# Kernel tuning notes

Hardware: AMD Instinct MI355X
Metric: run time of the kernel (lower is better)

The kernel has to match this reference:

```python
import jax, jax.numpy as jnp
import numpy as np


def _sobel(img):
    # replicate-pad then Sobel cross-correlation (matches torch conv2d with wx, wy)
    p = jnp.pad(img, ((0, 0), (0, 0), (1, 1), (1, 1)), mode='edge')
    dx = ((p[:, :, 0:-2, 2:] - p[:, :, 0:-2, 0:-2])
          + 2.0 * (p[:, :, 1:-1, 2:] - p[:, :, 1:-1, 0:-2])
          + (p[:, :, 2:, 2:] - p[:, :, 2:, 0:-2]))
    dy = ((p[:, :, 2:, 0:-2] - p[:, :, 0:-2, 0:-2])
          + 2.0 * (p[:, :, 2:, 1:-1] - p[:, :, 0:-2, 1:-1])
          + (p[:, :, 2:, 2:] - p[:, :, 0:-2, 2:]))
    return dx, dy


def _compute_normal(vertex):
    # normal = normalize(dV/dx x dV/dy); zero out pixels at global min/max depth
    dx, dy = _sobel(vertex)
    n = jnp.cross(dx, dy, axis=1)                      # [B,3,H,W]
    mag = jnp.sqrt(jnp.sum(n * n, axis=1, keepdims=True) + 1e-16)
    n = n / (mag + 1e-8)
    depth = vertex[:, 2:3]
    invalid = (depth == depth.min()) | (depth == depth.max())
    return jnp.where(invalid, 0.0, n)


def _warp(feat, u, v):
    # bilinear sampling of feat [B,C,H,W] at (u,v) [B,N] -> [B,C,N]
    B, C, H, W = feat.shape
    u = jnp.clip(u, 0.0, W - 1.0)
    v = jnp.clip(v, 0.0, H - 1.0)
    u0 = jnp.floor(u); v0 = jnp.floor(v)
    wu = u - u0; wv = v - v0
    u0i = u0.astype(jnp.int32); v0i = v0.astype(jnp.int32)
    u1i = jnp.minimum(u0i + 1, W - 1); v1i = jnp.minimum(v0i + 1, H - 1)
    flat = feat.reshape(B, C, H * W)
    N = u.shape[-1]
    def g(ui, vi):
        idx = (vi * W + ui)[:, None, :]
        return jnp.take_along_axis(flat, jnp.broadcast_to(idx, (B, C, N)), axis=2)
    return (g(u0i, v0i) * ((1 - wu) * (1 - wv))[:, None]
            + g(u1i, v0i) * (wu * (1 - wv))[:, None]
            + g(u0i, v1i) * ((1 - wu) * wv)[:, None]
            + g(u1i, v1i) * (wu * wv)[:, None])


def _skew(v):  # [B,3] -> [B,3,3]
    x, y, z = v[..., 0], v[..., 1], v[..., 2]
    O = jnp.zeros_like(x)
    return jnp.stack([jnp.stack([O, -z, y], -1),
                      jnp.stack([z, O, -x], -1),
                      jnp.stack([-y, x, O], -1)], -2)


def _twist2mat(w):  # Rodrigues: so(3) [B,3] -> SO(3) [B,3,3]
    th = jnp.sqrt(jnp.sum(w * w, -1, keepdims=True) + 1e-24)
    Kv = _skew(w / th)
    th = th[..., None]
    I = jnp.eye(3, dtype=w.dtype)
    return I + jnp.sin(th) * Kv + (1.0 - jnp.cos(th)) * (Kv @ Kv)


def _icp_forward(depth0, depth1, K, R, t, max_iter=3):
    B, _, H, W = depth0.shape
    fx, fy, cx, cy = [K[:, i:i + 1] for i in range(4)]  # each [B,1]
    uu = jnp.arange(W, dtype=depth0.dtype)
    vv = jnp.arange(H, dtype=depth0.dtype)
    px = (uu[None, None, None, :] - cx[:, :, None, None]) / fx[:, :, None, None]
    py = (vv[None, None, :, None] - cy[:, :, None, None]) / fy[:, :, None, None]
    px = jnp.broadcast_to(px, (B, 1, H, W))
    py = jnp.broadcast_to(py, (B, 1, H, W))
    vertex0 = jnp.concatenate([px * depth0, py * depth0, depth0], 1)  # [B,3,H,W]
    vertex1 = jnp.concatenate([px * depth1, py * depth1, depth1], 1)
    normal0 = _compute_normal(vertex0)
    normal1 = _compute_normal(vertex1)
    N = H * W
    V0 = vertex0.reshape(B, 3, N)
    N0 = normal0.reshape(B, 3, N)
    P0 = V0.transpose(0, 2, 1)                          # [B,N,3]
    dpt0 = vertex0[:, 2].reshape(B, N)
    sigma_z = 0.0012 + 0.0019 * (dpt0 - 0.4) ** 2       # depth noise model
    eye6 = jnp.eye(6, dtype=depth0.dtype)
    for _ in range(max_iter):
        v0to1 = R @ V0 + t                               # [B,3,N]
        x_, y_, s_ = v0to1[:, 0], v0to1[:, 1], v0to1[:, 2]
        u_ = x_ / s_ * fx + cx
        v_ = y_ / s_ * fy + cy
        inviews = (u_ > 0) & (u_ < W - 1) & (v_ > 0) & (v_ < H - 1)
        rV1 = _warp(vertex1, u_, v_)                     # [B,3,N]
        rN1 = _warp(normal1, u_, v_)
        diff = v0to1 - rV1
        dnorm = jnp.sqrt(jnp.sum(diff * diff, axis=1) + 1e-16)
        occ = (~inviews) | (dnorm > 0.1)                 # [B,N]
        res = jnp.sum(rN1 * diff, axis=1)                # point-to-plane residual [B,N]
        NtC = jnp.einsum('bcn,bck->bnk', rN1, R)         # n_r^T R, [B,N,3]
        # n^T [p]_x == cross(n^T R, p)
        J = jnp.concatenate([jnp.cross(NtC, P0), -NtC], -1)  # [B,N,6]
        # sigma ~ |n_r . (R e_z)| * sigma_z (depth noise projected on normal)
        ndot = jnp.abs(jnp.sum(rN1 * R[:, :, 2][:, :, None], axis=1))
        sigma = ndot * sigma_z + 1e-3
        w_res = res / (sigma + 1e-8)
        J = -J / (sigma + 1e-8)[..., None]
        w_res = jnp.where(occ, 0.0, w_res)
        J = jnp.where(occ[..., None], 0.0, J)
        JtWJ = jnp.einsum('bnk,bnl->bkl', J, J)          # [B,6,6]
        JtR = jnp.einsum('bnk,bn->bk', J, w_res)[..., None]  # [B,6,1]
        tr = jnp.trace(JtWJ, axis1=1, axis2=2)
        Hlm = JtWJ + (tr * 1e-6)[:, None, None] * eye6   # LM damping
        xi = jnp.linalg.inv(Hlm) @ JtR                   # [B,6,1]
        dR = _twist2mat(-xi[:, :3, 0])
        dt = -(dR @ xi[:, 3:])
        R, t = R @ dR, R @ dt + t                        # inverse-compositional update
    weights = jnp.ones((B, 1, H, W), dtype=depth0.dtype)
    return R, t, weights


def setup_inputs() -> dict:
    key = jax.random.key(0)
    B, H, W = 16, 480, 640
    k1, k2, k3, k4 = jax.random.split(key, 4)
    TWO_PI = 6.2831853
    xs = jnp.linspace(0.0, 1.0, W, dtype=jnp.float32)
    ys = jnp.linspace(0.0, 1.0, H, dtype=jnp.float32)
    phase = jax.random.uniform(k1, (B, 1, 1, 1), minval=0.0, maxval=TWO_PI)
    # smooth positive depth surface so ICP inlier test keeps valid pixels
    depth0 = (2.0 + 0.5 * jnp.sin(TWO_PI * 3.0 * xs[None, None, None, :] + phase)
              * jnp.cos(TWO_PI * 2.0 * ys[None, None, :, None])).astype(jnp.float32)
    depth1 = depth0 + 0.01 * jax.random.normal(k2, (B, 1, H, W), dtype=jnp.float32)
    K = jnp.tile(jnp.array([[525.0, 525.0, 319.5, 239.5]], dtype=jnp.float32), (B, 1))
    w = 0.005 * jax.random.normal(k3, (B, 3), dtype=jnp.float32)
    R = _twist2mat(w)                                    # near-identity initial rotation
    t = 0.005 * jax.random.normal(k4, (B, 3, 1), dtype=jnp.float32)
    return {"depth0": depth0, "depth1": depth1, "K": K, "R": R, "t": t}


def reference(depth0, depth1, K, R, t):
    return _icp_forward(depth0, depth1, K, R, t, max_iter=3)
```

## Files before the change

### kernel.cpp

```cpp
#include <hip/hip_runtime.h>
#include <hip/hip_fp16.h>

#define IMH 480
#define IMW 640
#define HW (IMH*IMW)
#define NB 16

#define BPB 100
#define TPX 4
#define GROUPS 3
#define THREADS_PB (BPB*256)
#define GSTRIDE (THREADS_PB*TPX)
#define GROWS (GSTRIDE/IMW)

__device__ inline unsigned fenc(float x){
    unsigned u = __float_as_uint(x);
    return (u & 0x80000000u) ? ~u : (u | 0x80000000u);
}
__device__ inline float fdec(unsigned e){
    unsigned u = (e & 0x80000000u) ? (e & 0x7FFFFFFFu) : ~e;
    return __uint_as_float(u);
}

__global__ void init_kernel(const float* __restrict__ Rin, const float* __restrict__ tin,
                            float* __restrict__ stateR, float* __restrict__ statet,
                            unsigned* __restrict__ mm, float* __restrict__ acc){
    int i = threadIdx.x;
    if (i < NB*9) stateR[i] = Rin[i];
    if (i < NB*3) statet[i] = tin[i];
    if (i == 0){ mm[0] = 0xFFFFFFFFu; mm[1] = 0u; }
    for (int k = i; k < NB*27; k += 256) acc[k] = 0.f;
}

__global__ __launch_bounds__(256) void minmax_kernel(const float4* __restrict__ d, unsigned* __restrict__ mm){
    unsigned lmin = 0xFFFFFFFFu, lmax = 0u;
    const int total4 = NB*HW/4;
    for (int i = blockIdx.x*256 + threadIdx.x; i < total4; i += gridDim.x*256){
        float4 v = d[i];
        unsigned e0 = fenc(v.x), e1 = fenc(v.y), e2 = fenc(v.z), e3 = fenc(v.w);
        lmin = min(lmin, min(min(e0,e1), min(e2,e3)));
        lmax = max(lmax, max(max(e0,e1), max(e2,e3)));
    }
    #pragma unroll
    for (int off = 32; off; off >>= 1){
        lmin = min(lmin, (unsigned)__shfl_down((int)lmin, off));
        lmax = max(lmax, (unsigned)__shfl_down((int)lmax, off));
    }
    __shared__ unsigned smin[4], smax[4];
    int wave = threadIdx.x >> 6, lane = threadIdx.x & 63;
    if (lane == 0){ smin[wave] = lmin; smax[wave] = lmax; }
    __syncthreads();
    if (threadIdx.x == 0){
        unsigned bmin = min(min(smin[0],smin[1]), min(smin[2],smin[3]));
        unsigned bmax = max(max(smax[0],smax[1]), max(smax[2],smax[3]));
        atomicMin(&mm[0], bmin);
        atomicMax(&mm[1], bmax);
    }
}

__global__ __launch_bounds__(256) void normal_kernel(const float* __restrict__ depth1,
                                                     const float* __restrict__ Kp,
                                                     const unsigned* __restrict__ mm,
                                                     uint2* __restrict__ nrm,
                                                     float* __restrict__ weights){
    int b = blockIdx.y;
    int pix = blockIdx.x*256 + threadIdx.x;
    int r = pix / IMW, c = pix % IMW;
    const float fx = Kp[b*4+0], fy = Kp[b*4+1], cx = Kp[b*4+2], cy = Kp[b*4+3];
    const float inv_fx = 1.f/fx, inv_fy = 1.f/fy;
    const float* __restrict__ d = depth1 + (size_t)b*HW;
    int rm = max(r-1,0), rp = min(r+1,IMH-1), cm = max(c-1,0), cp = min(c+1,IMW-1);

    auto vert = [&](int rr, int cc, float v[3]){
        float dd = d[rr*IMW+cc];
        v[0] = ((float)cc - cx)*inv_fx*dd;
        v[1] = ((float)rr - cy)*inv_fy*dd;
        v[2] = dd;
    };
    float va[3],vb[3],vc2[3],vd[3],ve[3],vf[3],vg[3],vh[3];
    vert(rm,cm,va); vert(rm,c,vb);  vert(rm,cp,vc2);
    vert(r ,cm,vd);                 vert(r ,cp,ve);
    vert(rp,cm,vf); vert(rp,c,vg);  vert(rp,cp,vh);

    float dx[3], dy[3];
    #pragma unroll
    for (int k=0;k<3;k++){
        dx[k] = (vc2[k]-va[k]) + 2.f*(ve[k]-vd[k]) + (vh[k]-vf[k]);
        dy[k] = (vf[k]-va[k]) + 2.f*(vg[k]-vb[k]) + (vh[k]-vc2[k]);
    }
    float nx = dx[1]*dy[2] - dx[2]*dy[1];
    float ny = dx[2]*dy[0] - dx[0]*dy[2];
    float nz = dx[0]*dy[1] - dx[1]*dy[0];
    float mag = sqrtf(nx*nx + ny*ny + nz*nz + 1e-16f);
    float inv = __builtin_amdgcn_rcpf(mag + 1e-8f);
    nx *= inv; ny *= inv; nz *= inv;

    float dc = d[r*IMW+c];
    float dmin = fdec(mm[0]), dmax = fdec(mm[1]);
    if (dc == dmin || dc == dmax){ nx = 0.f; ny = 0.f; nz = 0.f; }

    __half2 hxy = __floats2half2_rn(nx, ny);
    __half2 hz0 = __floats2half2_rn(nz, 0.f);
    uint2 p;
    p.x = *reinterpret_cast<unsigned*>(&hxy);
    p.y = *reinterpret_cast<unsigned*>(&hz0);
    nrm[(size_t)b*HW + pix] = p;
    weights[(size_t)b*HW + pix] = 1.f;
}

__global__ __launch_bounds__(256) void iter_kernel(const float4* __restrict__ depth0_v4,
                                                   const float* __restrict__ depth1,
                                                   const uint2* __restrict__ nrm,
                                                   const float* __restrict__ Kp,
                                                   const float* __restrict__ stateR,
                                                   const float* __restrict__ statet,
                                                   float* __restrict__ acc){
    const int b = blockIdx.y;
    const float fx = Kp[b*4+0], fy = Kp[b*4+1], cx = Kp[b*4+2], cy = Kp[b*4+3];
    const float inv_fx = 1.f/fx, inv_fy = 1.f/fy;
    float Rm[9];
    #pragma unroll
    for (int i=0;i<9;i++) Rm[i] = stateR[b*9+i];
    float tv[3];
    #pragma unroll
    for (int i=0;i<3;i++) tv[i] = statet[b*3+i];

    const float4* __restrict__ d0v = depth0_v4 + (size_t)b*(HW/4);
    const float* __restrict__ d1   = depth1 + (size_t)b*HW;
    const uint2* __restrict__ nb_  = nrm + (size_t)b*HW;

    float accv[27];
    #pragma unroll
    for (int i=0;i<27;i++) accv[i] = 0.f;

    const int tid = blockIdx.x*256 + threadIdx.x;
    const int base0 = tid*TPX;
    const int c0 = base0 % IMW;
    const int r0 = base0 / IMW;
    const float px_base = ((float)c0 - cx)*inv_fx;
    float pyv = ((float)r0 - cy)*inv_fy;
    const float py_step = (float)GROWS*inv_fy;

    #pragma unroll 1
    for (int g = 0; g < GROUPS; g++){
        float4 d4 = d0v[tid + g*THREADS_PB];
        float dd[4] = {d4.x, d4.y, d4.z, d4.w};

        #pragma unroll
        for (int j = 0; j < TPX; j++){
            float d0 = dd[j];
            float V0x = (px_base + (float)j*inv_fx)*d0;
            float V0y = pyv*d0;
            float V0z = d0;

            float X = Rm[0]*V0x + Rm[1]*V0y + Rm[2]*V0z + tv[0];
            float Y = Rm[3]*V0x + Rm[4]*V0y + Rm[5]*V0z + tv[1];
            float Z = Rm[6]*V0x + Rm[7]*V0y + Rm[8]*V0z + tv[2];
            float invZ = __builtin_amdgcn_rcpf(Z);
            float uu = X*invZ*fx + cx;
            float vv = Y*invZ*fy + cy;

            bool inview = (uu > 0.f) && (uu < (float)(IMW-1)) && (vv > 0.f) && (vv < (float)(IMH-1));

            float J0=0.f,J1=0.f,J2=0.f,J3=0.f,J4=0.f,J5=0.f,wres=0.f;
            if (inview){
                float u0f = floorf(uu), v0f = floorf(vv);
                int u0 = (int)u0f, v0 = (int)v0f;
                float wu = uu - u0f, wv = vv - v0f;
                float w00 = (1.f-wu)*(1.f-wv), w10 = wu*(1.f-wv), w01 = (1.f-wu)*wv, w11 = wu*wv;
                int i00 = v0*IMW + u0;

                float d00 = d1[i00], d10 = d1[i00+1], d01 = d1[i00+IMW], d11 = d1[i00+IMW+1];
                uint2 h00 = nb_[i00], h10 = nb_[i00+1], h01 = nb_[i00+IMW], h11 = nb_[i00+IMW+1];

                float pxa = (u0f - cx)*inv_fx, pxb = pxa + inv_fx;
                float pya = (v0f - cy)*inv_fy, pyb = pya + inv_fy;
                float a = w00*d00, bb = w10*d10, cc = w01*d01, ee = w11*d11;
                float rVz = (a + bb) + (cc + ee);
                float rVx = (a + cc)*pxa + (bb + ee)*pxb;
                float rVy = (a + bb)*pya + (cc + ee)*pyb;

                float2 n00xy = __half22float2(*reinterpret_cast<__half2*>(&h00.x));
                float2 n00z_ = __half22float2(*reinterpret_cast<__half2*>(&h00.y));
                float2 n10xy = __half22float2(*reinterpret_cast<__half2*>(&h10.x));
                float2 n10z_ = __half22float2(*reinterpret_cast<__half2*>(&h10.y));
                float2 n01xy = __half22float2(*reinterpret_cast<__half2*>(&h01.x));
                float2 n01z_ = __half22float2(*reinterpret_cast<__half2*>(&h01.y));
                float2 n11xy = __half22float2(*reinterpret_cast<__half2*>(&h11.x));
                float2 n11z_ = __half22float2(*reinterpret_cast<__half2*>(&h11.y));

                float n0x = w00*n00xy.x + w10*n10xy.x + w01*n01xy.x + w11*n11xy.x;
                float n0y = w00*n00xy.y + w10*n10xy.y + w01*n01xy.y + w11*n11xy.y;
                float n0z = w00*n00z_.x + w10*n10z_.x + w01*n01z_.x + w11*n11z_.x;

                float dfx = X - rVx, dfy = Y - rVy, dfz = Z - rVz;
                float d2 = dfx*dfx + dfy*dfy + dfz*dfz + 1e-16f;
                if (d2 <= 0.01f){
                    float res = n0x*dfx + n0y*dfy + n0z*dfz;
                    float N0 = n0x*Rm[0] + n0y*Rm[3] + n0z*Rm[6];
                    float N1 = n0x*Rm[1] + n0y*Rm[4] + n0z*Rm[7];
                    float N2 = n0x*Rm[2] + n0y*Rm[5] + n0z*Rm[8];
                    float cr0 = N1*V0z - N2*V0y;
                    float cr1 = N2*V0x - N0*V0z;
                    float cr2 = N0*V0y - N1*V0x;
                    float ndot = fabsf(N2);
                    float dsh = d0 - 0.4f;
                    float sigz = 0.0012f + 0.0019f*dsh*dsh;
                    float sigma = ndot*sigz + 0.001f;
                    float invs = __builtin_amdgcn_rcpf(sigma + 1e-8f);
                    wres = res*invs;
                    J0 = -cr0*invs; J1 = -cr1*invs; J2 = -cr2*invs;
                    J3 =  N0*invs;  J4 =  N1*invs;  J5 =  N2*invs;
                }
            }

            float Jv[6] = {J0,J1,J2,J3,J4,J5};
            int idx = 0;
            #pragma unroll
            for (int k=0;k<6;k++)
                #pragma unroll
                for (int l=k;l<6;l++){ accv[idx] += Jv[k]*Jv[l]; idx++; }
            #pragma unroll
            for (int k=0;k<6;k++){ accv[idx] += Jv[k]*wres; idx++; }
        }

        pyv += py_step;
    }

    #pragma unroll
    for (int i=0;i<27;i++){
        float v = accv[i];
        #pragma unroll
        for (int off=32; off; off >>= 1) v += __shfl_down(v, off);
        accv[i] = v;
    }

    __shared__ float sacc[4][27];
    int wave = threadIdx.x >> 6, lane = threadIdx.x & 63;
    if (lane == 0){
        #pragma unroll
        for (int i=0;i<27;i++) sacc[wave][i] = accv[i];
    }
    __syncthreads();
    if (threadIdx.x < 27){
        float s = sacc[0][threadIdx.x] + sacc[1][threadIdx.x]
                + sacc[2][threadIdx.x] + sacc[3][threadIdx.x];
        atomicAdd(&acc[b*27 + threadIdx.x], s);
    }
}

__global__ void solve_kernel(float* __restrict__ acc,
                             float* __restrict__ stateR, float* __restrict__ statet,
                             float* __restrict__ outR, float* __restrict__ outt){
    int b = threadIdx.x;
    if (b >= NB) return;

    float a27[27];
    #pragma unroll
    for (int i=0;i<27;i++) a27[i] = acc[b*27+i];
    #pragma unroll
    for (int i=0;i<27;i++) acc[b*27+i] = 0.f;

    float A[6][6], rhs[6];
    int idx = 0;
    #pragma unroll
    for (int k=0;k<6;k++)
        #pragma unroll
        for (int l=k;l<6;l++){ A[k][l] = a27[idx]; A[l][k] = a27[idx]; idx++; }
    #pragma unroll
    for (int k=0;k<6;k++) rhs[k] = a27[21+k];

    float tr = 0.f;
    #pragma unroll
    for (int k=0;k<6;k++) tr += A[k][k];
    float lm = tr*1e-6f;
    #pragma unroll
    for (int k=0;k<6;k++) A[k][k] += lm;

    float L[6][6];
    #pragma unroll
    for (int i=0;i<6;i++){
        #pragma unroll
        for (int j=0;j<=i;j++){
            float s = A[i][j];
            #pragma unroll
            for (int k=0;k<j;k++) s -= L[i][k]*L[j][k];
            if (i == j) L[i][i] = sqrtf(s);
            else        L[i][j] = s / L[j][j];
        }
    }
    float y[6];
    #pragma unroll
    for (int i=0;i<6;i++){
        float s = rhs[i];
        #pragma unroll
        for (int k=0;k<i;k++) s -= L[i][k]*y[k];
        y[i] = s / L[i][i];
    }
    float xi[6];
    #pragma unroll
    for (int ii=5; ii>=0; ii--){
        float s = y[ii];
        #pragma unroll
        for (int k=ii+1;k<6;k++) s -= L[k][ii]*xi[k];
        xi[ii] = s / L[ii][ii];
    }

    float w0 = -xi[0], w1 = -xi[1], w2 = -xi[2];
    float th = sqrtf(w0*w0 + w1*w1 + w2*w2 + 1e-24f);
    float ith = 1.f/th;
    float kx = w0*ith, ky = w1*ith, kz = w2*ith;
    float s = sinf(th), cm1 = 1.f - cosf(th);
    float dRm[9];
    dRm[0] = 1.f + cm1*(-ky*ky - kz*kz);
    dRm[1] = -s*kz + cm1*(kx*ky);
    dRm[2] =  s*ky + cm1*(kx*kz);
    dRm[3] =  s*kz + cm1*(kx*ky);
    dRm[4] = 1.f + cm1*(-kx*kx - kz*kz);
    dRm[5] = -s*kx + cm1*(ky*kz);
    dRm[6] = -s*ky + cm1*(kx*kz);
    dRm[7] =  s*kx + cm1*(ky*kz);
    dRm[8] = 1.f + cm1*(-kx*kx - ky*ky);

    float dt0 = -(dRm[0]*xi[3] + dRm[1]*xi[4] + dRm[2]*xi[5]);
    float dt1 = -(dRm[3]*xi[3] + dRm[4]*xi[4] + dRm[5]*xi[5]);
    float dt2 = -(dRm[6]*xi[3] + dRm[7]*xi[4] + dRm[8]*xi[5]);

    float Rm[9], tv[3];
    #pragma unroll
    for (int i=0;i<9;i++) Rm[i] = stateR[b*9+i];
    #pragma unroll
    for (int i=0;i<3;i++) tv[i] = statet[b*3+i];

    float Rn[9];
    #pragma unroll
    for (int i=0;i<3;i++)
        #pragma unroll
        for (int j=0;j<3;j++)
            Rn[i*3+j] = Rm[i*3+0]*dRm[0*3+j] + Rm[i*3+1]*dRm[1*3+j] + Rm[i*3+2]*dRm[2*3+j];
    float tn0 = Rm[0]*dt0 + Rm[1]*dt1 + Rm[2]*dt2 + tv[0];
    float tn1 = Rm[3]*dt0 + Rm[4]*dt1 + Rm[5]*dt2 + tv[1];
    float tn2 = Rm[6]*dt0 + Rm[7]*dt1 + Rm[8]*dt2 + tv[2];

    #pragma unroll
    for (int i=0;i<9;i++){ stateR[b*9+i] = Rn[i]; outR[b*9+i] = Rn[i]; }
    statet[b*3+0] = tn0; outt[b*3+0] = tn0;
    statet[b*3+1] = tn1; outt[b*3+1] = tn1;
    statet[b*3+2] = tn2; outt[b*3+2] = tn2;
}

extern "C" void kernel_launch(void* const* d_in, const int* in_sizes, int n_in,
                              void* d_out, int out_size, void* d_ws, size_t ws_size,
                              hipStream_t stream){
    const float* depth0 = (const float*)d_in[0];
    const float* depth1 = (const float*)d_in[1];
    const float* Kp     = (const float*)d_in[2];
    const float* Rin    = (const float*)d_in[3];
    const float* tin    = (const float*)d_in[4];

    float* out     = (float*)d_out;
    float* outR    = out;
    float* outt    = out + NB*9;
    float* weights = out + NB*12;

    uint2* nrm     = (uint2*)d_ws;
    float* stateR  = (float*)(nrm + (size_t)NB*HW);
    float* statet  = stateR + NB*9;
    unsigned* mm   = (unsigned*)(statet + NB*3);
    float* acc     = (float*)(mm + 2);

    init_kernel<<<1, 256, 0, stream>>>(Rin, tin, stateR, statet, mm, acc);
    minmax_kernel<<<dim3(512), 256, 0, stream>>>((const float4*)depth1, mm);
    normal_kernel<<<dim3(HW/256, NB), 256, 0, stream>>>(depth1, Kp, mm, nrm, weights);
    for (int it = 0; it < 3; it++){
        iter_kernel<<<dim3(BPB, NB), 256, 0, stream>>>((const float4*)depth0, depth1, nrm, Kp, stateR, statet, acc);
        solve_kernel<<<1, 64, 0, stream>>>(acc, stateR, statet, outR, outt);
    }
}
```

Measured before the change: 245.9 us.

## Use per-thread strided pixel mapping and DPP wave reduction in ICP iteration

Measured after the change: 267.0 us. 8.6% more time.

```diff
diff --git a/kernel.cpp b/kernel.cpp
--- a/kernel.cpp
+++ b/kernel.cpp
@@ -7,11 +7,10 @@
 #define NB 16
 
 #define BPB 100
-#define TPX 4
+#define THREADS_PB (BPB*256)
+#define CH_ROWS (THREADS_PB/IMW)
+#define NCH 12
 #define GROUPS 3
-#define THREADS_PB (BPB*256)
-#define GSTRIDE (THREADS_PB*TPX)
-#define GROWS (GSTRIDE/IMW)
 
 __device__ inline unsigned fenc(float x){
     unsigned u = __float_as_uint(x);
@@ -20,6 +19,16 @@
 __device__ inline float fdec(unsigned e){
     unsigned u = (e & 0x80000000u) ? (e & 0x7FFFFFFFu) : ~e;
     return __uint_as_float(u);
+}
+
+__device__ inline float wave_sum_dpp(float x){
+    x += __int_as_float(__builtin_amdgcn_update_dpp(0, __float_as_int(x), 0x111, 0xf, 0xf, true));
+    x += __int_as_float(__builtin_amdgcn_update_dpp(0, __float_as_int(x), 0x112, 0xf, 0xf, true));
+    x += __int_as_float(__builtin_amdgcn_update_dpp(0, __float_as_int(x), 0x114, 0xf, 0xf, true));
+    x += __int_as_float(__builtin_amdgcn_update_dpp(0, __float_as_int(x), 0x118, 0xf, 0xf, true));
+    x += __int_as_float(__builtin_amdgcn_update_dpp(0, __float_as_int(x), 0x142, 0xf, 0xf, true));
+    x += __int_as_float(__builtin_amdgcn_update_dpp(0, __float_as_int(x), 0x143, 0xf, 0xf, true));
+    return x;
 }
 
 __global__ void init_kernel(const float* __restrict__ Rin, const float* __restrict__ tin,
@@ -108,7 +117,7 @@
     weights[(size_t)b*HW + pix] = 1.f;
 }
 
-__global__ __launch_bounds__(256) void iter_kernel(const float4* __restrict__ depth0_v4,
+__global__ __launch_bounds__(256) void iter_kernel(const float* __restrict__ depth0,
                                                    const float* __restrict__ depth1,
                                                    const uint2* __restrict__ nrm,
                                                    const float* __restrict__ Kp,
@@ -125,31 +134,31 @@
     #pragma unroll
     for (int i=0;i<3;i++) tv[i] = statet[b*3+i];
 
-    const float4* __restrict__ d0v = depth0_v4 + (size_t)b*(HW/4);
-    const float* __restrict__ d1   = depth1 + (size_t)b*HW;
-    const uint2* __restrict__ nb_  = nrm + (size_t)b*HW;
+    const float* __restrict__ d0p = depth0 + (size_t)b*HW;
+    const float* __restrict__ d1  = depth1 + (size_t)b*HW;
+    const uint2* __restrict__ nb_ = nrm + (size_t)b*HW;
 
     float accv[27];
     #pragma unroll
     for (int i=0;i<27;i++) accv[i] = 0.f;
 
     const int tid = blockIdx.x*256 + threadIdx.x;
-    const int base0 = tid*TPX;
-    const int c0 = base0 % IMW;
-    const int r0 = base0 / IMW;
-    const float px_base = ((float)c0 - cx)*inv_fx;
-    float pyv = ((float)r0 - cy)*inv_fy;
-    const float py_step = (float)GROWS*inv_fy;
+    const int c0  = tid % IMW;
+    const int r0  = tid / IMW;
+    const float px0 = ((float)c0 - cx)*inv_fx;
+    const float py0 = ((float)r0 - cy)*inv_fy;
+    const float py_step = (float)CH_ROWS*inv_fy;
 
     #pragma unroll 1
     for (int g = 0; g < GROUPS; g++){
-        float4 d4 = d0v[tid + g*THREADS_PB];
-        float dd[4] = {d4.x, d4.y, d4.z, d4.w};
-
-        #pragma unroll
-        for (int j = 0; j < TPX; j++){
-            float d0 = dd[j];
-            float V0x = (px_base + (float)j*inv_fx)*d0;
+        #pragma unroll
+        for (int j = 0; j < 4; j++){
+            const int k = g*4 + j;
+            const int pix = tid + k*THREADS_PB;
+            float d0 = d0p[pix];
+            float pyv = py0 + (float)k*py_step;
+
+            float V0x = px0*d0;
             float V0y = pyv*d0;
             float V0z = d0;
 
@@ -217,27 +226,20 @@
             float Jv[6] = {J0,J1,J2,J3,J4,J5};
             int idx = 0;
             #pragma unroll
-            for (int k=0;k<6;k++)
+            for (int k2=0;k2<6;k2++)
                 #pragma unroll
-                for (int l=k;l<6;l++){ accv[idx] += Jv[k]*Jv[l]; idx++; }
+                for (int l=k2;l<6;l++){ accv[idx] += Jv[k2]*Jv[l]; idx++; }
             #pragma unroll
-            for (int k=0;k<6;k++){ accv[idx] += Jv[k]*wres; idx++; }
+            for (int k2=0;k2<6;k2++){ accv[idx] += Jv[k2]*wres; idx++; }
         }
-
-        pyv += py_step;
-    }
-
-    #pragma unroll
-    for (int i=0;i<27;i++){
-        float v = accv[i];
-        #pragma unroll
-        for (int off=32; off; off >>= 1) v += __shfl_down(v, off);
-        accv[i] = v;
-    }
+    }
+
+    #pragma unroll
+    for (int i=0;i<27;i++) accv[i] = wave_sum_dpp(accv[i]);
 
     __shared__ float sacc[4][27];
     int wave = threadIdx.x >> 6, lane = threadIdx.x & 63;
-    if (lane == 0){
+    if (lane == 63){
         #pragma unroll
         for (int i=0;i<27;i++) sacc[wave][i] = accv[i];
     }
@@ -370,10 +372,10 @@
     float* acc     = (float*)(mm + 2);
 
     init_kernel<<<1, 256, 0, stream>>>(Rin, tin, stateR, statet, mm, acc);
-    minmax_kernel<<<dim3(512), 256, 0, stream>>>((const float4*)depth1, mm);
+    minmax_kernel<<<dim3(1024), 256, 0, stream>>>((const float4*)depth1, mm);
     normal_kernel<<<dim3(HW/256, NB), 256, 0, stream>>>(depth1, Kp, mm, nrm, weights);
     for (int it = 0; it < 3; it++){
-        iter_kernel<<<dim3(BPB, NB), 256, 0, stream>>>((const float4*)depth0, depth1, nrm, Kp, stateR, statet, acc);
+        iter_kernel<<<dim3(BPB, NB), 256, 0, stream>>>(depth0, depth1, nrm, Kp, stateR, statet, acc);
         solve_kernel<<<1, 64, 0, stream>>>(acc, stateR, statet, outR, outt);
     }
 }
```
